# Kernel optimization log

Measured on AMD Instinct MI355X. Metric: run time of the kernel, lower is better.

Reference implementation:

```python
import jax, jax.numpy as jnp
import numpy as np

B = 256   # batch size; must equal N for the module's final broadcast to be valid
N = 256   # num feature vectors per sample
D = 1024  # feature dim
S = 1024  # state dim


def setup_inputs() -> dict:
    key = jax.random.key(0)
    k1, k2, k3, k4 = jax.random.split(key, 4)
    return {
        "feature_vectors": jax.random.normal(k1, (B, N, D), dtype=jnp.float32),
        "state_output": jax.random.normal(k2, (B, S), dtype=jnp.float32),
        # tf.random_normal_initializer default stddev=0.05
        "Q": 0.05 * jax.random.normal(k3, (S, S), dtype=jnp.float32),
        "K": 0.05 * jax.random.normal(k4, (S, N), dtype=jnp.float32),
    }


def reference(feature_vectors, state_output, Q, K):
    # Loop body: ((Q @ state^T)^T @ K) @ feature_vectors[i]
    # (Q @ state^T)^T == state @ Q^T  -> [B, S]
    A = state_output @ Q.T            # [B, S]
    M = A @ K                         # [B, N]
    # stack over i: W[i, b, d] = sum_n M[b, n] * FV[i, n, d]
    W = jnp.einsum('bn,ind->ibd', M, feature_vectors)   # [B, B, D]
    W = jax.nn.softmax(W, axis=-1)
    # broadcast multiply [B, B, D] * [B, N(=B), D], sum over axis=1
    context_vector = jnp.sum(W * feature_vectors, axis=1)  # [B, D]
    return (context_vector, W)
```

## Files before the change

### kernel.cpp

```cpp
#include <hip/hip_runtime.h>


typedef _Float16 half8 __attribute__((ext_vector_type(8)));
typedef float floatx16 __attribute__((ext_vector_type(16)));

static __device__ __forceinline__ void split_f32(float x, _Float16& hi, _Float16& lo) {
    _Float16 h = (_Float16)x;
    hi = h;
    lo = (_Float16)(x - (float)h);
}

template <bool BT, bool OUT_HILO>
__global__ __launch_bounds__(256, 2) void gemm_small(
    const float* __restrict__ Ag, const float* __restrict__ Bg,
    float* __restrict__ Cf, _Float16* __restrict__ Chi, _Float16* __restrict__ Clo,
    int Kdim, int Ndim)
{
    __shared__ __align__(16) _Float16 AsHi[4 * 64 * 8];
    __shared__ __align__(16) _Float16 AsLo[4 * 64 * 8];
    __shared__ __align__(16) _Float16 BsHi[4 * 64 * 8];
    __shared__ __align__(16) _Float16 BsLo[4 * 64 * 8];

    const int tid  = threadIdx.x;
    const int lane = tid & 63;
    const int wave = tid >> 6;
    const int wy = wave >> 1, wx = wave & 1;
    const int l31 = lane & 31, l5 = lane >> 5;
    const int m0 = blockIdx.y * 64, n0 = blockIdx.x * 64;

    floatx16 acc;
#pragma unroll
    for (int j = 0; j < 16; ++j) acc[j] = 0.0f;

    const int sA_m  = tid >> 2;
    const int sA_kg = tid & 3;
    const int sB_n  = tid & 63;
    const int sB_kg = tid >> 6;

    const int nkt = Kdim / 32;
#pragma unroll 1
    for (int kt = 0; kt < nkt; ++kt) {
        __syncthreads();
        {
            const float* src = Ag + (size_t)(m0 + sA_m) * Kdim + kt * 32 + sA_kg * 8;
            half8 hi, lo;
#pragma unroll
            for (int j = 0; j < 8; ++j) {
                _Float16 h, l;
                split_f32(src[j], h, l);
                hi[j] = h; lo[j] = l;
            }
            *(half8*)&AsHi[(sA_kg * 64 + sA_m) * 8] = hi;
            *(half8*)&AsLo[(sA_kg * 64 + sA_m) * 8] = lo;
        }
        if constexpr (BT) {
            const float* src = Bg + (size_t)(n0 + sA_m) * Kdim + kt * 32 + sA_kg * 8;
            half8 hi, lo;
#pragma unroll
            for (int j = 0; j < 8; ++j) {
                _Float16 h, l;
                split_f32(src[j], h, l);
                hi[j] = h; lo[j] = l;
            }
            *(half8*)&BsHi[(sA_kg * 64 + sA_m) * 8] = hi;
            *(half8*)&BsLo[(sA_kg * 64 + sA_m) * 8] = lo;
        } else {
            const float* src = Bg + (size_t)(kt * 32 + sB_kg * 8) * Ndim + n0 + sB_n;
            half8 hi, lo;
#pragma unroll
            for (int j = 0; j < 8; ++j) {
                _Float16 h, l;
                split_f32(src[(size_t)j * Ndim], h, l);
                hi[j] = h; lo[j] = l;
            }
            *(half8*)&BsHi[(sB_kg * 64 + sB_n) * 8] = hi;
            *(half8*)&BsLo[(sB_kg * 64 + sB_n) * 8] = lo;
        }
        __syncthreads();
#pragma unroll
        for (int ks = 0; ks < 2; ++ks) {
            const int kg = ks * 2 + l5;
            const half8 ah = *(half8*)&AsHi[(kg * 64 + wy * 32 + l31) * 8];
            const half8 al = *(half8*)&AsLo[(kg * 64 + wy * 32 + l31) * 8];
            const half8 bh = *(half8*)&BsHi[(kg * 64 + wx * 32 + l31) * 8];
            const half8 bl = *(half8*)&BsLo[(kg * 64 + wx * 32 + l31) * 8];
            acc = __builtin_amdgcn_mfma_f32_32x32x16_f16(ah, bh, acc, 0, 0, 0);
            acc = __builtin_amdgcn_mfma_f32_32x32x16_f16(ah, bl, acc, 0, 0, 0);
            acc = __builtin_amdgcn_mfma_f32_32x32x16_f16(al, bh, acc, 0, 0, 0);
        }
    }

#pragma unroll
    for (int reg = 0; reg < 16; ++reg) {
        const int row = m0 + wy * 32 + (reg & 3) + 8 * (reg >> 2) + 4 * l5;
        const int col = n0 + wx * 32 + l31;
        const float v = acc[reg];
        if constexpr (OUT_HILO) {
            _Float16 h, l;
            split_f32(v, h, l);
            Chi[(size_t)row * Ndim + col] = h;
            Clo[(size_t)row * Ndim + col] = l;
        } else {
            Cf[(size_t)row * Ndim + col] = v;
        }
    }
}

__global__ __launch_bounds__(512, 2) void fused_attn(
    const float* __restrict__ FV, const _Float16* __restrict__ Mhi,
    const _Float16* __restrict__ Mlo, float* __restrict__ ctx,
    float* __restrict__ Wout)
{
    __shared__ __align__(16) _Float16 AsHi[2 * 64 * 8];
    __shared__ __align__(16) _Float16 AsLo[2 * 64 * 8];
    __shared__ __align__(16) _Float16 Bs[2 * 1024 * 8];
    __shared__ __align__(16) float red1[64 * 4];
    __shared__ __align__(16) float red2[64 * 4];

    const int tid  = threadIdx.x;
    const int lane = tid & 63;
    const int wave = tid >> 6;
    const int wx = wave & 3;
    const int wy = wave >> 2;
    const int l31 = lane & 31, l5 = lane >> 5;

    const int w   = blockIdx.x;
    const int xcd = w & 7;
    const int k   = w >> 3;
    const int i   = (xcd << 5) + (k >> 2);
    const int bt  = k & 3;

    const float* __restrict__ FVi = FV + (size_t)i * 256 * 1024;

    floatx16 acc[8];
#pragma unroll
    for (int nt = 0; nt < 8; ++nt)
#pragma unroll
        for (int j = 0; j < 16; ++j) acc[nt][j] = 0.0f;

    const int am = tid >> 1, akg = tid & 1;

    float pv[4][8];
    half8 pah, pal;
#pragma unroll
    for (int rep = 0; rep < 4; ++rep) {
        const int q8 = rep >> 1;
        const int d  = (rep & 1) * 512 + tid;
        const float* src = FVi + (size_t)(q8 * 8) * 1024 + d;
#pragma unroll
        for (int r = 0; r < 8; ++r) pv[rep][r] = src[(size_t)r * 1024];
    }
    if (tid < 128) {
        pah = *(const half8*)(Mhi + (size_t)(bt * 64 + am) * 256 + akg * 8);
        pal = *(const half8*)(Mlo + (size_t)(bt * 64 + am) * 256 + akg * 8);
    }

#pragma unroll 1
    for (int kt = 0; kt < 16; ++kt) {
        __syncthreads();
        if (tid < 128) {
            *(half8*)&AsHi[(akg * 64 + am) * 8] = pah;
            *(half8*)&AsLo[(akg * 64 + am) * 8] = pal;
        }
#pragma unroll
        for (int rep = 0; rep < 4; ++rep) {
            const int q8 = rep >> 1;
            const int d  = (rep & 1) * 512 + tid;
            half8 h;
#pragma unroll
            for (int r = 0; r < 8; ++r) h[r] = (_Float16)pv[rep][r];
            *(half8*)&Bs[(q8 * 1024 + d) * 8] = h;
        }
        __syncthreads();
        if (kt + 1 < 16) {
#pragma unroll
            for (int rep = 0; rep < 4; ++rep) {
                const int q8 = rep >> 1;
                const int d  = (rep & 1) * 512 + tid;
                const float* src = FVi + (size_t)((kt + 1) * 16 + q8 * 8) * 1024 + d;
#pragma unroll
                for (int r = 0; r < 8; ++r) pv[rep][r] = src[(size_t)r * 1024];
            }
            if (tid < 128) {
                pah = *(const half8*)(Mhi + (size_t)(bt * 64 + am) * 256 + (kt + 1) * 16 + akg * 8);
                pal = *(const half8*)(Mlo + (size_t)(bt * 64 + am) * 256 + (kt + 1) * 16 + akg * 8);
            }
        }
        const half8 ah = *(half8*)&AsHi[(l5 * 64 + wy * 32 + l31) * 8];
        const half8 al = *(half8*)&AsLo[(l5 * 64 + wy * 32 + l31) * 8];
#pragma unroll
        for (int nt = 0; nt < 8; ++nt) {
            const half8 b = *(half8*)&Bs[(l5 * 1024 + wx * 256 + nt * 32 + l31) * 8];
            acc[nt] = __builtin_amdgcn_mfma_f32_32x32x16_f16(ah, b, acc[nt], 0, 0, 0);
            acc[nt] = __builtin_amdgcn_mfma_f32_32x32x16_f16(al, b, acc[nt], 0, 0, 0);
        }
    }

    float st[16];
#pragma unroll
    for (int reg = 0; reg < 16; ++reg) {
        float v = acc[0][reg];
#pragma unroll
        for (int nt = 1; nt < 8; ++nt) v = fmaxf(v, acc[nt][reg]);
#pragma unroll
        for (int off = 1; off < 32; off <<= 1) v = fmaxf(v, __shfl_xor(v, off));
        st[reg] = v;
    }
    if (l31 == 0) {
#pragma unroll
        for (int reg = 0; reg < 16; ++reg) {
            const int row = wy * 32 + (reg & 3) + 8 * (reg >> 2) + 4 * l5;
            red1[row * 4 + wx] = st[reg];
        }
    }
    __syncthreads();
    float rmax[16];
#pragma unroll
    for (int reg = 0; reg < 16; ++reg) {
        const int row = wy * 32 + (reg & 3) + 8 * (reg >> 2) + 4 * l5;
        const float4 m4 = *(const float4*)&red1[row * 4];
        rmax[reg] = fmaxf(fmaxf(m4.x, m4.y), fmaxf(m4.z, m4.w));
    }
#pragma unroll
    for (int reg = 0; reg < 16; ++reg) {
        float s = 0.0f;
#pragma unroll
        for (int nt = 0; nt < 8; ++nt) {
            const float p = __expf(acc[nt][reg] - rmax[reg]);
            acc[nt][reg] = p;
            s += p;
        }
#pragma unroll
        for (int off = 1; off < 32; off <<= 1) s += __shfl_xor(s, off);
        st[reg] = s;
    }
    if (l31 == 0) {
#pragma unroll
        for (int reg = 0; reg < 16; ++reg) {
            const int row = wy * 32 + (reg & 3) + 8 * (reg >> 2) + 4 * l5;
            red2[row * 4 + wx] = st[reg];
        }
    }
    __syncthreads();
    float inv[16];
#pragma unroll
    for (int reg = 0; reg < 16; ++reg) {
        const int row = wy * 32 + (reg & 3) + 8 * (reg >> 2) + 4 * l5;
        const float4 s4 = *(const float4*)&red2[row * 4];
        inv[reg] = 1.0f / (s4.x + s4.y + s4.z + s4.w);
    }

    float csum[8];
#pragma unroll
    for (int nt = 0; nt < 8; ++nt) csum[nt] = 0.0f;

    const int rowbase = bt * 64 + wy * 32;
#pragma unroll
    for (int nt = 0; nt < 8; ++nt) {
        const int col = wx * 256 + nt * 32 + l31;
#pragma unroll
        for (int reg = 0; reg < 16; ++reg) {
            const int row = (reg & 3) + 8 * (reg >> 2) + 4 * l5;
            const float w = acc[nt][reg] * inv[reg];
            Wout[((size_t)(i * 256 + rowbase + row)) * 1024 + col] = w;
            const float fv = FVi[(size_t)(rowbase + row) * 1024 + col];
            csum[nt] += w * fv;
        }
    }
#pragma unroll
    for (int nt = 0; nt < 8; ++nt) {
        const float v = csum[nt] + __shfl_xor(csum[nt], 32);
        if (l5 == 0)
            atomicAdd(&ctx[(size_t)i * 1024 + wx * 256 + nt * 32 + l31], v);
    }
}

extern "C" void kernel_launch(void* const* d_in, const int* in_sizes, int n_in,
                              void* d_out, int out_size, void* d_ws, size_t ws_size,
                              hipStream_t stream)
{
    const float* FV    = (const float*)d_in[0];
    const float* state = (const float*)d_in[1];
    const float* Q     = (const float*)d_in[2];
    const float* Km    = (const float*)d_in[3];

    float* out = (float*)d_out;
    float* ctx = out;
    float* W   = out + 256 * 1024;

    char* ws = (char*)d_ws;
    float*    A1  = (float*)ws;
    _Float16* Mhi = (_Float16*)(ws + (1 << 20));
    _Float16* Mlo = (_Float16*)(ws + (1 << 20) + (1 << 17));

    (void)hipMemsetAsync(ctx, 0, 256 * 1024 * sizeof(float), stream);

    gemm_small<true, false><<<dim3(16, 4), 256, 0, stream>>>(
        state, Q, A1, nullptr, nullptr, 1024, 1024);

    gemm_small<false, true><<<dim3(4, 4), 256, 0, stream>>>(
        A1, Km, nullptr, Mhi, Mlo, 1024, 256);

    fused_attn<<<dim3(1024), 512, 0, stream>>>(FV, Mhi, Mlo, ctx, W);
}
```

Baseline: 649.2 us.

## Shrink fused attention tile to 32 rows and drop register prefetch for occupancy

The fused softmax-attention kernel now gives each block 32 output rows instead of 64, with all 8 waves laid out along the D dimension, and launches 2048 blocks. The register-held prefetch of the next FV and M tiles is removed, so loads happen directly before the LDS store. Accumulator registers are halved, which lets launch bounds ask for 4 blocks per CU and use occupancy to hide latency. In exchange, FV tiles are loaded and converted twice as often per sample (each row block rereads the whole FV slice), and the software pipelining is lost.

```diff
diff --git a/kernel.cpp b/kernel.cpp
--- a/kernel.cpp
+++ b/kernel.cpp
@@ -106,172 +106,144 @@
     }
 }
 
-__global__ __launch_bounds__(512, 2) void fused_attn(
+__global__ __launch_bounds__(512, 4) void fused_attn(
     const float* __restrict__ FV, const _Float16* __restrict__ Mhi,
     const _Float16* __restrict__ Mlo, float* __restrict__ ctx,
     float* __restrict__ Wout)
 {
-    __shared__ __align__(16) _Float16 AsHi[2 * 64 * 8];
-    __shared__ __align__(16) _Float16 AsLo[2 * 64 * 8];
+    __shared__ __align__(16) _Float16 AsHi[2 * 32 * 8];
+    __shared__ __align__(16) _Float16 AsLo[2 * 32 * 8];
     __shared__ __align__(16) _Float16 Bs[2 * 1024 * 8];
-    __shared__ __align__(16) float red1[64 * 4];
-    __shared__ __align__(16) float red2[64 * 4];
+    __shared__ __align__(16) float red1[32 * 8];
+    __shared__ __align__(16) float red2[32 * 8];
 
     const int tid  = threadIdx.x;
     const int lane = tid & 63;
     const int wave = tid >> 6;
-    const int wx = wave & 3;
-    const int wy = wave >> 2;
+    const int wx = wave;
     const int l31 = lane & 31, l5 = lane >> 5;
 
     const int w   = blockIdx.x;
     const int xcd = w & 7;
     const int k   = w >> 3;
-    const int i   = (xcd << 5) + (k >> 2);
-    const int bt  = k & 3;
+    const int i   = (xcd << 5) + (k >> 3);
+    const int bt  = k & 7;
 
     const float* __restrict__ FVi = FV + (size_t)i * 256 * 1024;
 
-    floatx16 acc[8];
-#pragma unroll
-    for (int nt = 0; nt < 8; ++nt)
+    floatx16 acc[4];
+#pragma unroll
+    for (int nt = 0; nt < 4; ++nt)
 #pragma unroll
         for (int j = 0; j < 16; ++j) acc[nt][j] = 0.0f;
 
     const int am = tid >> 1, akg = tid & 1;
-
-    float pv[4][8];
-    half8 pah, pal;
-#pragma unroll
-    for (int rep = 0; rep < 4; ++rep) {
-        const int q8 = rep >> 1;
-        const int d  = (rep & 1) * 512 + tid;
-        const float* src = FVi + (size_t)(q8 * 8) * 1024 + d;
-#pragma unroll
-        for (int r = 0; r < 8; ++r) pv[rep][r] = src[(size_t)r * 1024];
-    }
-    if (tid < 128) {
-        pah = *(const half8*)(Mhi + (size_t)(bt * 64 + am) * 256 + akg * 8);
-        pal = *(const half8*)(Mlo + (size_t)(bt * 64 + am) * 256 + akg * 8);
-    }
 
 #pragma unroll 1
     for (int kt = 0; kt < 16; ++kt) {
         __syncthreads();
-        if (tid < 128) {
-            *(half8*)&AsHi[(akg * 64 + am) * 8] = pah;
-            *(half8*)&AsLo[(akg * 64 + am) * 8] = pal;
+        if (tid < 64) {
+            const half8 h = *(const half8*)(Mhi + (size_t)(bt * 32 + am) * 256 + kt * 16 + akg * 8);
+            const half8 l = *(const half8*)(Mlo + (size_t)(bt * 32 + am) * 256 + kt * 16 + akg * 8);
+            *(half8*)&AsHi[(akg * 32 + am) * 8] = h;
+            *(half8*)&AsLo[(akg * 32 + am) * 8] = l;
         }
 #pragma unroll
         for (int rep = 0; rep < 4; ++rep) {
             const int q8 = rep >> 1;
             const int d  = (rep & 1) * 512 + tid;
+            const float* src = FVi + (size_t)(kt * 16 + q8 * 8) * 1024 + d;
             half8 h;
 #pragma unroll
-            for (int r = 0; r < 8; ++r) h[r] = (_Float16)pv[rep][r];
+            for (int r = 0; r < 8; ++r) h[r] = (_Float16)src[(size_t)r * 1024];
             *(half8*)&Bs[(q8 * 1024 + d) * 8] = h;
         }
         __syncthreads();
-        if (kt + 1 < 16) {
-#pragma unroll
-            for (int rep = 0; rep < 4; ++rep) {
-                const int q8 = rep >> 1;
-                const int d  = (rep & 1) * 512 + tid;
-                const float* src = FVi + (size_t)((kt + 1) * 16 + q8 * 8) * 1024 + d;
-#pragma unroll
-                for (int r = 0; r < 8; ++r) pv[rep][r] = src[(size_t)r * 1024];
-            }
-            if (tid < 128) {
-                pah = *(const half8*)(Mhi + (size_t)(bt * 64 + am) * 256 + (kt + 1) * 16 + akg * 8);
-                pal = *(const half8*)(Mlo + (size_t)(bt * 64 + am) * 256 + (kt + 1) * 16 + akg * 8);
-            }
-        }
-        const half8 ah = *(half8*)&AsHi[(l5 * 64 + wy * 32 + l31) * 8];
-        const half8 al = *(half8*)&AsLo[(l5 * 64 + wy * 32 + l31) * 8];
-#pragma unroll
-        for (int nt = 0; nt < 8; ++nt) {
-            const half8 b = *(half8*)&Bs[(l5 * 1024 + wx * 256 + nt * 32 + l31) * 8];
+        const half8 ah = *(half8*)&AsHi[(l5 * 32 + l31) * 8];
+        const half8 al = *(half8*)&AsLo[(l5 * 32 + l31) * 8];
+#pragma unroll
+        for (int nt = 0; nt < 4; ++nt) {
+            const half8 b = *(half8*)&Bs[(l5 * 1024 + wx * 128 + nt * 32 + l31) * 8];
             acc[nt] = __builtin_amdgcn_mfma_f32_32x32x16_f16(ah, b, acc[nt], 0, 0, 0);
             acc[nt] = __builtin_amdgcn_mfma_f32_32x32x16_f16(al, b, acc[nt], 0, 0, 0);
         }
     }
 
-    float st[16];
-#pragma unroll
-    for (int reg = 0; reg < 16; ++reg) {
-        float v = acc[0][reg];
-#pragma unroll
-        for (int nt = 1; nt < 8; ++nt) v = fmaxf(v, acc[nt][reg]);
-#pragma unroll
-        for (int off = 1; off < 32; off <<= 1) v = fmaxf(v, __shfl_xor(v, off));
-        st[reg] = v;
-    }
-    if (l31 == 0) {
+    {
+        float st[16];
 #pragma unroll
         for (int reg = 0; reg < 16; ++reg) {
-            const int row = wy * 32 + (reg & 3) + 8 * (reg >> 2) + 4 * l5;
-            red1[row * 4 + wx] = st[reg];
+            float v = acc[0][reg];
+#pragma unroll
+            for (int nt = 1; nt < 4; ++nt) v = fmaxf(v, acc[nt][reg]);
+#pragma unroll
+            for (int off = 1; off < 32; off <<= 1) v = fmaxf(v, __shfl_xor(v, off));
+            st[reg] = v;
+        }
+        if (l31 == 0) {
+#pragma unroll
+            for (int reg = 0; reg < 16; ++reg) {
+                const int row = (reg & 3) + 8 * (reg >> 2) + 4 * l5;
+                red1[row * 8 + wx] = st[reg];
+            }
         }
     }
     __syncthreads();
-    float rmax[16];
-#pragma unroll
-    for (int reg = 0; reg < 16; ++reg) {
-        const int row = wy * 32 + (reg & 3) + 8 * (reg >> 2) + 4 * l5;
-        const float4 m4 = *(const float4*)&red1[row * 4];
-        rmax[reg] = fmaxf(fmaxf(m4.x, m4.y), fmaxf(m4.z, m4.w));
-    }
-#pragma unroll
-    for (int reg = 0; reg < 16; ++reg) {
-        float s = 0.0f;
-#pragma unroll
-        for (int nt = 0; nt < 8; ++nt) {
-            const float p = __expf(acc[nt][reg] - rmax[reg]);
-            acc[nt][reg] = p;
-            s += p;
-        }
-#pragma unroll
-        for (int off = 1; off < 32; off <<= 1) s += __shfl_xor(s, off);
-        st[reg] = s;
-    }
-    if (l31 == 0) {
-#pragma unroll
-        for (int reg = 0; reg < 16; ++reg) {
-            const int row = wy * 32 + (reg & 3) + 8 * (reg >> 2) + 4 * l5;
-            red2[row * 4 + wx] = st[reg];
-        }
-    }
-    __syncthreads();
-    float inv[16];
-#pragma unroll
-    for (int reg = 0; reg < 16; ++reg) {
-        const int row = wy * 32 + (reg & 3) + 8 * (reg >> 2) + 4 * l5;
-        const float4 s4 = *(const float4*)&red2[row * 4];
-        inv[reg] = 1.0f / (s4.x + s4.y + s4.z + s4.w);
-    }
-
-    float csum[8];
-#pragma unroll
-    for (int nt = 0; nt < 8; ++nt) csum[nt] = 0.0f;
-
-    const int rowbase = bt * 64 + wy * 32;
-#pragma unroll
-    for (int nt = 0; nt < 8; ++nt) {
-        const int col = wx * 256 + nt * 32 + l31;
+    {
+        float st[16];
 #pragma unroll
         for (int reg = 0; reg < 16; ++reg) {
             const int row = (reg & 3) + 8 * (reg >> 2) + 4 * l5;
-            const float w = acc[nt][reg] * inv[reg];
-            Wout[((size_t)(i * 256 + rowbase + row)) * 1024 + col] = w;
+            const float4 a4 = *(const float4*)&red1[row * 8];
+            const float4 b4 = *(const float4*)&red1[row * 8 + 4];
+            const float rmax = fmaxf(fmaxf(fmaxf(a4.x, a4.y), fmaxf(a4.z, a4.w)),
+                                     fmaxf(fmaxf(b4.x, b4.y), fmaxf(b4.z, b4.w)));
+            float s = 0.0f;
+#pragma unroll
+            for (int nt = 0; nt < 4; ++nt) {
+                const float p = __expf(acc[nt][reg] - rmax);
+                acc[nt][reg] = p;
+                s += p;
+            }
+#pragma unroll
+            for (int off = 1; off < 32; off <<= 1) s += __shfl_xor(s, off);
+            st[reg] = s;
+        }
+        if (l31 == 0) {
+#pragma unroll
+            for (int reg = 0; reg < 16; ++reg) {
+                const int row = (reg & 3) + 8 * (reg >> 2) + 4 * l5;
+                red2[row * 8 + wx] = st[reg];
+            }
+        }
+    }
+    __syncthreads();
+
+    float csum[4];
+#pragma unroll
+    for (int nt = 0; nt < 4; ++nt) csum[nt] = 0.0f;
+
+    const int rowbase = bt * 32;
+#pragma unroll
+    for (int nt = 0; nt < 4; ++nt) {
+        const int col = wx * 128 + nt * 32 + l31;
+#pragma unroll
+        for (int reg = 0; reg < 16; ++reg) {
+            const int row = (reg & 3) + 8 * (reg >> 2) + 4 * l5;
+            const float4 a4 = *(const float4*)&red2[row * 8];
+            const float4 b4 = *(const float4*)&red2[row * 8 + 4];
+            const float inv = 1.0f / (a4.x + a4.y + a4.z + a4.w + b4.x + b4.y + b4.z + b4.w);
+            const float wv = acc[nt][reg] * inv;
+            Wout[((size_t)(i * 256 + rowbase + row)) * 1024 + col] = wv;
             const float fv = FVi[(size_t)(rowbase + row) * 1024 + col];
-            csum[nt] += w * fv;
-        }
-    }
-#pragma unroll
-    for (int nt = 0; nt < 8; ++nt) {
+            csum[nt] += wv * fv;
+        }
+    }
+#pragma unroll
+    for (int nt = 0; nt < 4; ++nt) {
         const float v = csum[nt] + __shfl_xor(csum[nt], 32);
         if (l5 == 0)
-            atomicAdd(&ctx[(size_t)i * 1024 + wx * 256 + nt * 32 + l31], v);
+            atomicAdd(&ctx[(size_t)i * 1024 + wx * 128 + nt * 32 + l31], v);
     }
 }
 
@@ -301,5 +273,5 @@
     gemm_small<false, true><<<dim3(4, 4), 256, 0, stream>>>(
         A1, Km, nullptr, Mhi, Mlo, 1024, 256);
 
-    fused_attn<<<dim3(1024), 512, 0, stream>>>(FV, Mhi, Mlo, ctx, W);
-}
+    fused_attn<<<dim3(2048), 512, 0, stream>>>(FV, Mhi, Mlo, ctx, W);
+}
```

New measurement: 1.411 ms. 117% more time.

## Load MFMA operands directly from global memory, dropping LDS staging and barriers

Applied to the files above, without the earlier changes.

The fused attention kernel no longer stages the M tiles and fp16-converted feature-vector tiles through shared memory with register prefetch and two barriers per k-step. Each wave now loads its A fragments and the fp32 feature values straight from global memory and converts them to fp16 in registers before the MFMAs. This removes LDS traffic and synchronisation, but each wave's loads are no longer prefetched ahead of use, so latency is exposed. The wy=0 and wy=1 waves sharing a column slice now each read the same feature values, relying on cache. The variable rename in the epilogue is cosmetic.

```diff
diff --git a/kernel.cpp b/kernel.cpp
--- a/kernel.cpp
+++ b/kernel.cpp
@@ -111,9 +111,6 @@
     const _Float16* __restrict__ Mlo, float* __restrict__ ctx,
     float* __restrict__ Wout)
 {
-    __shared__ __align__(16) _Float16 AsHi[2 * 64 * 8];
-    __shared__ __align__(16) _Float16 AsLo[2 * 64 * 8];
-    __shared__ __align__(16) _Float16 Bs[2 * 1024 * 8];
     __shared__ __align__(16) float red1[64 * 4];
     __shared__ __align__(16) float red2[64 * 4];
 
@@ -138,59 +135,22 @@
 #pragma unroll
         for (int j = 0; j < 16; ++j) acc[nt][j] = 0.0f;
 
-    const int am = tid >> 1, akg = tid & 1;
-
-    float pv[4][8];
-    half8 pah, pal;
-#pragma unroll
-    for (int rep = 0; rep < 4; ++rep) {
-        const int q8 = rep >> 1;
-        const int d  = (rep & 1) * 512 + tid;
-        const float* src = FVi + (size_t)(q8 * 8) * 1024 + d;
-#pragma unroll
-        for (int r = 0; r < 8; ++r) pv[rep][r] = src[(size_t)r * 1024];
-    }
-    if (tid < 128) {
-        pah = *(const half8*)(Mhi + (size_t)(bt * 64 + am) * 256 + akg * 8);
-        pal = *(const half8*)(Mlo + (size_t)(bt * 64 + am) * 256 + akg * 8);
-    }
+    const int arow = bt * 64 + wy * 32 + l31;
+    const _Float16* __restrict__ Ah = Mhi + (size_t)arow * 256 + l5 * 8;
+    const _Float16* __restrict__ Al = Mlo + (size_t)arow * 256 + l5 * 8;
+    const float* __restrict__ Bbase = FVi + (size_t)(l5 * 8) * 1024 + wx * 256 + l31;
 
 #pragma unroll 1
     for (int kt = 0; kt < 16; ++kt) {
-        __syncthreads();
-        if (tid < 128) {
-            *(half8*)&AsHi[(akg * 64 + am) * 8] = pah;
-            *(half8*)&AsLo[(akg * 64 + am) * 8] = pal;
-        }
-#pragma unroll
-        for (int rep = 0; rep < 4; ++rep) {
-            const int q8 = rep >> 1;
-            const int d  = (rep & 1) * 512 + tid;
-            half8 h;
-#pragma unroll
-            for (int r = 0; r < 8; ++r) h[r] = (_Float16)pv[rep][r];
-            *(half8*)&Bs[(q8 * 1024 + d) * 8] = h;
-        }
-        __syncthreads();
-        if (kt + 1 < 16) {
-#pragma unroll
-            for (int rep = 0; rep < 4; ++rep) {
-                const int q8 = rep >> 1;
-                const int d  = (rep & 1) * 512 + tid;
-                const float* src = FVi + (size_t)((kt + 1) * 16 + q8 * 8) * 1024 + d;
-#pragma unroll
-                for (int r = 0; r < 8; ++r) pv[rep][r] = src[(size_t)r * 1024];
-            }
-            if (tid < 128) {
-                pah = *(const half8*)(Mhi + (size_t)(bt * 64 + am) * 256 + (kt + 1) * 16 + akg * 8);
-                pal = *(const half8*)(Mlo + (size_t)(bt * 64 + am) * 256 + (kt + 1) * 16 + akg * 8);
-            }
-        }
-        const half8 ah = *(half8*)&AsHi[(l5 * 64 + wy * 32 + l31) * 8];
-        const half8 al = *(half8*)&AsLo[(l5 * 64 + wy * 32 + l31) * 8];
+        const half8 ah = *(const half8*)(Ah + kt * 16);
+        const half8 al = *(const half8*)(Al + kt * 16);
+        const float* bp = Bbase + (size_t)kt * 16 * 1024;
 #pragma unroll
         for (int nt = 0; nt < 8; ++nt) {
-            const half8 b = *(half8*)&Bs[(l5 * 1024 + wx * 256 + nt * 32 + l31) * 8];
+            half8 b;
+#pragma unroll
+            for (int r = 0; r < 8; ++r)
+                b[r] = (_Float16)bp[nt * 32 + (size_t)r * 1024];
             acc[nt] = __builtin_amdgcn_mfma_f32_32x32x16_f16(ah, b, acc[nt], 0, 0, 0);
             acc[nt] = __builtin_amdgcn_mfma_f32_32x32x16_f16(al, b, acc[nt], 0, 0, 0);
         }
@@ -261,10 +221,10 @@
 #pragma unroll
         for (int reg = 0; reg < 16; ++reg) {
             const int row = (reg & 3) + 8 * (reg >> 2) + 4 * l5;
-            const float w = acc[nt][reg] * inv[reg];
-            Wout[((size_t)(i * 256 + rowbase + row)) * 1024 + col] = w;
+            const float wv = acc[nt][reg] * inv[reg];
+            Wout[((size_t)(i * 256 + rowbase + row)) * 1024 + col] = wv;
             const float fv = FVi[(size_t)(rowbase + row) * 1024 + col];
-            csum[nt] += w * fv;
+            csum[nt] += wv * fv;
         }
     }
 #pragma unroll
```

New measurement: 662.8 us. 1.02x slower.
